# Performance work log

Hardware: AMD Instinct MI355X
Metric: run time of the kernel (lower is better)

## Reference

```python
import jax, jax.numpy as jnp
import numpy as np

B = 65536
T = 512
DT = 0.01  # time-grid spacing


def setup_inputs() -> dict:
    key = jax.random.key(0)
    k1, k2 = jax.random.split(key)
    y0 = jax.random.normal(k1, (B, 3), dtype=jnp.float32)
    t_span = jnp.arange(T, dtype=jnp.float32) * DT
    params = jax.random.uniform(k2, (B, 3), dtype=jnp.float32)
    return {"y0": y0, "t_span": t_span, "params": params}


def _bloch_rhs_incomplete(y, params):
    # y: [B,3] -> (u, v, w); params: [B,3] -> Omega = params[:,0], gamma = params[:,2]
    u = y[:, 0:1]
    v = y[:, 1:2]
    w = y[:, 2:3]
    Omega = params[:, 0:1]
    gamma = params[:, 2:3]
    du = -gamma * u
    dv = -gamma * v - Omega * w
    dw = -2.0 * gamma * (w + 1.0) + Omega * v
    return jnp.concatenate([du, dv, dw], axis=-1)


def reference(y0, t_span, params):
    dts = t_span[1:] - t_span[:-1]  # [T-1]

    def rk4_step(y, dt):
        k1 = _bloch_rhs_incomplete(y, params)
        k2 = _bloch_rhs_incomplete(y + 0.5 * dt * k1, params)
        k3 = _bloch_rhs_incomplete(y + 0.5 * dt * k2, params)
        k4 = _bloch_rhs_incomplete(y + dt * k3, params)
        y_new = y + dt / 6.0 * (k1 + 2.0 * k2 + 2.0 * k3 + k4)
        return y_new, y_new

    _, ys = jax.lax.scan(rk4_step, y0, dts)  # ys: [T-1, B, 3]
    return jnp.concatenate([y0[None], ys], axis=0)  # [T, B, 3]
```

## Files before the change

kernel.cpp:

```cpp
#include <hip/hip_runtime.h>


#define NB 65536
#define NT 512

__global__ __launch_bounds__(256) void bloch_rk4_kernel(
    const float* __restrict__ y0,
    const float* __restrict__ tspan,
    const float* __restrict__ params,
    float* __restrict__ out)
{
    __shared__ float sdt[NT];
    const int tid = threadIdx.x;
    for (int i = tid; i < NT; i += 256) {
        float d = 0.0f;
        if (i < NT - 1) d = tspan[i + 1] - tspan[i];
        sdt[i] = d;
    }
    __syncthreads();

    const int b   = blockIdx.x * 256 + tid;
    const int ib3 = b * 3;

    float u = y0[ib3 + 0];
    float v = y0[ib3 + 1];
    float w = y0[ib3 + 2];
    const float Om = params[ib3 + 0];
    const float g  = params[ib3 + 2];
    const float g2 = 2.0f * g;

    out[ib3 + 0] = u;
    out[ib3 + 1] = v;
    out[ib3 + 2] = w;

    float dt = sdt[0];
    for (int i = 1; i < NT; ++i) {
        const float dt_next = sdt[i];

        const float k1u = -g * u;
        const float k1v = -g * v - Om * w;
        const float k1w = Om * v - g2 * w - g2;

        const float h = 0.5f * dt;
        float uu = u + h * k1u;
        float vv = v + h * k1v;
        float ww = w + h * k1w;

        const float k2u = -g * uu;
        const float k2v = -g * vv - Om * ww;
        const float k2w = Om * vv - g2 * ww - g2;

        uu = u + h * k2u;
        vv = v + h * k2v;
        ww = w + h * k2w;

        const float k3u = -g * uu;
        const float k3v = -g * vv - Om * ww;
        const float k3w = Om * vv - g2 * ww - g2;

        uu = u + dt * k3u;
        vv = v + dt * k3v;
        ww = w + dt * k3w;

        const float k4u = -g * uu;
        const float k4v = -g * vv - Om * ww;
        const float k4w = Om * vv - g2 * ww - g2;

        const float s = dt * (1.0f / 6.0f);
        u += s * (k1u + 2.0f * k2u + 2.0f * k3u + k4u);
        v += s * (k1v + 2.0f * k2v + 2.0f * k3v + k4v);
        w += s * (k1w + 2.0f * k2w + 2.0f * k3w + k4w);

        const size_t o = (size_t)i * (NB * 3) + (size_t)ib3;
        out[o + 0] = u;
        out[o + 1] = v;
        out[o + 2] = w;

        dt = dt_next;
    }
}

extern "C" void kernel_launch(void* const* d_in, const int* in_sizes, int n_in,
                              void* d_out, int out_size, void* d_ws, size_t ws_size,
                              hipStream_t stream) {
    const float* y0     = (const float*)d_in[0];
    const float* tspan  = (const float*)d_in[1];
    const float* params = (const float*)d_in[2];
    float* out = (float*)d_out;

    bloch_rk4_kernel<<<NB / 256, 256, 0, stream>>>(y0, tspan, params, out);
}
```

Baseline: 403.0 us.

## Stage outputs in double-buffered shared memory for coalesced float4 stores

Each thread now writes its (u,v,w) result into a shared-memory staging buffer covering four time steps. Every fourth step the block syncs and writes the staged data to global memory as contiguous float4 stores. This replaces strided 3-float per-thread stores and is meant to improve write coalescing on a store-bound kernel. In exchange it adds a block barrier every four steps and 24KB of shared memory per block, which may reduce occupancy.

```diff
diff --git a/kernel.cpp b/kernel.cpp
--- a/kernel.cpp
+++ b/kernel.cpp
@@ -3,6 +3,7 @@
 
 #define NB 65536
 #define NT 512
+#define B3 (NB * 3)
 
 __global__ __launch_bounds__(256) void bloch_rk4_kernel(
     const float* __restrict__ y0,
@@ -11,6 +12,8 @@
     float* __restrict__ out)
 {
     __shared__ float sdt[NT];
+    __shared__ float buf[2][4 * 768];
+
     const int tid = threadIdx.x;
     for (int i = tid; i < NT; i += 256) {
         float d = 0.0f;
@@ -19,7 +22,8 @@
     }
     __syncthreads();
 
-    const int b   = blockIdx.x * 256 + tid;
+    const int S   = blockIdx.x * 256;
+    const int b   = S + tid;
     const int ib3 = b * 3;
 
     float u = y0[ib3 + 0];
@@ -29,13 +33,15 @@
     const float g  = params[ib3 + 2];
     const float g2 = 2.0f * g;
 
-    out[ib3 + 0] = u;
-    out[ib3 + 1] = v;
-    out[ib3 + 2] = w;
+    int p = 0;
+    {
+        float* bp = &buf[p][tid * 3];
+        bp[0] = u; bp[1] = v; bp[2] = w;
+    }
 
     float dt = sdt[0];
-    for (int i = 1; i < NT; ++i) {
-        const float dt_next = sdt[i];
+    for (int t = 1; t < NT; ++t) {
+        const float dt_next = sdt[t];
 
         const float k1u = -g * u;
         const float k1v = -g * v - Om * w;
@@ -66,15 +72,31 @@
         const float k4v = -g * vv - Om * ww;
         const float k4w = Om * vv - g2 * ww - g2;
 
-        const float s = dt * (1.0f / 6.0f);
-        u += s * (k1u + 2.0f * k2u + 2.0f * k3u + k4u);
-        v += s * (k1v + 2.0f * k2v + 2.0f * k3v + k4v);
-        w += s * (k1w + 2.0f * k2w + 2.0f * k3w + k4w);
+        const float s6 = dt * (1.0f / 6.0f);
+        u += s6 * (k1u + 2.0f * k2u + 2.0f * k3u + k4u);
+        v += s6 * (k1v + 2.0f * k2v + 2.0f * k3v + k4v);
+        w += s6 * (k1w + 2.0f * k2w + 2.0f * k3w + k4w);
 
-        const size_t o = (size_t)i * (NB * 3) + (size_t)ib3;
-        out[o + 0] = u;
-        out[o + 1] = v;
-        out[o + 2] = w;
+        const int s = t & 3;
+        {
+            float* bp = &buf[p][s * 768 + tid * 3];
+            bp[0] = u; bp[1] = v; bp[2] = w;
+        }
+
+        if (s == 3) {
+            __syncthreads();
+            const float4* src = (const float4*)buf[p];
+            const int t0 = t - 3;
+            #pragma unroll
+            for (int k = 0; k < 3; ++k) {
+                const int j  = tid + k * 256;
+                const int ss = j / 192;
+                const int r  = j - ss * 192;
+                float4* dst = (float4*)(out + (size_t)(t0 + ss) * B3 + S * 3);
+                dst[r] = src[j];
+            }
+            p ^= 1;
+        }
 
         dt = dt_next;
     }
```

Result: slower. 438.4 us (+8.8%).
